# Optimization experiments

Hardware: AMD Instinct MI355X
Metric: run time of the kernel (lower is better)

Reference implementation:

```python
import jax, jax.numpy as jnp
import numpy as np

B, T, D = 128, 2048, 256
LAMDA = 0.5


def setup_inputs() -> dict:
    key = jax.random.key(0)
    ks = jax.random.split(key, 8)
    return {
        "sentiment": jax.random.normal(ks[0], (B, D), jnp.float32),
        "aspect": jax.random.normal(ks[1], (B, D), jnp.float32),
        "sentiment_memory": jax.random.normal(ks[2], (B, T, D), jnp.float32),
        "aspect_memory": jax.random.normal(ks[3], (B, T, D), jnp.float32),
        "mask": jnp.ones((B, T), jnp.float32),
        # MultiplicativeAttention params: rand(D,D)*0.2-0.1, bias zeros(1)
        "W_mul": jax.random.uniform(ks[4], (D, D), jnp.float32) * 0.2 - 0.1,
        "b_mul": jnp.zeros((1,), jnp.float32),
        # AdditiveAttention: Linear(2D, 1) -> weight vector [2D], bias [1]
        "w_ss": jax.random.normal(ks[5], (2 * D,), jnp.float32) * 0.02,
        "b_ss": jnp.zeros((1,), jnp.float32),
        "w_sa": jax.random.normal(ks[6], (2 * D,), jnp.float32) * 0.02,
        "b_sa": jnp.zeros((1,), jnp.float32),
    }


def _masked_norm(scores, mask):
    # exp(scores - max) * mask, normalized (matches torch branch exactly)
    s = scores - jnp.max(scores, axis=1, keepdims=True)
    e = jnp.exp(s) * mask
    return e / jnp.sum(e, axis=1, keepdims=True)


def _additive_attn(query, key_mem, w, b, mask):
    # Linear([key; query_repeated]) == key @ w_k + query @ w_q + b
    d = query.shape[-1]
    scores = key_mem @ w[:d] + (query @ w[d:])[:, None] + b[0]  # [B,T]
    return _masked_norm(scores, mask)


def reference(sentiment, aspect, sentiment_memory, aspect_memory, mask,
              W_mul, b_mul, w_ss, b_ss, w_sa, b_sa):
    # Multiplicative attention over aspect_memory (no mask -> plain softmax)
    mids = aspect @ W_mul.T                                        # W @ q, [B,D]
    a_scores = jnp.tanh(jnp.einsum('btd,bd->bt', aspect_memory, mids) + b_mul[0])
    aspect_attn = jax.nn.softmax(a_scores, axis=1)                 # [B,T]
    new_aspect = jnp.einsum('bt,btd->bd', aspect_attn, aspect_memory)  # [B,D]

    ss_attn = _additive_attn(sentiment, sentiment_memory, w_ss, b_ss, mask)
    sa_attn = _additive_attn(new_aspect, sentiment_memory, w_sa, b_sa, mask)
    s_attn = (1.0 - LAMDA) * ss_attn + LAMDA * sa_attn             # [B,T]

    sentiment_out = jnp.einsum('bt,btd->bd', s_attn, sentiment_memory)[:, None, :]  # [B,1,D]
    aspect_out = aspect + new_aspect                                # [B,D]
    return sentiment_out, aspect_out
```

## Files before the change

### kernel.cpp

```cpp
#include <hip/hip_runtime.h>
#include <math.h>

#define BB 128
#define TT 2048
#define DD 256
#define SPLIT 8
#define ROWS_PER_BLOCK (TT / SPLIT)
#define WAVES 4
#define ROWS_PER_WAVE (ROWS_PER_BLOCK / WAVES)

#define WS_MIDS 0
#define WS_P1ACC (WS_MIDS + BB * DD)
#define WS_P1SUM (WS_P1ACC + BB * SPLIT * DD)
#define WS_P2ACC_SS (WS_P1SUM + BB * SPLIT)
#define WS_P2ACC_SA (WS_P2ACC_SS + BB * SPLIT * DD)
#define WS_P2SUM_SS (WS_P2ACC_SA + BB * SPLIT * DD)
#define WS_P2SUM_SA (WS_P2SUM_SS + BB * SPLIT)

__device__ __forceinline__ float wave_reduce_add(float v) {
    #pragma unroll
    for (int off = 32; off > 0; off >>= 1)
        v += __shfl_xor(v, off, 64);
    return v;
}

__device__ __forceinline__ float dot4(const float4& a, const float4& b) {
    return a.x * b.x + a.y * b.y + a.z * b.z + a.w * b.w;
}

__device__ __forceinline__ float tanh_fast(float x) {
    float ax = fabsf(x);
    float t = __expf(-2.0f * ax);
    float th = (1.0f - t) / (1.0f + t);
    return copysignf(th, x);
}

__global__ __launch_bounds__(DD) void mids_kernel(
    const float* __restrict__ aspect, const float* __restrict__ W,
    float* __restrict__ ws)
{
    const int b = blockIdx.x;
    const int i = threadIdx.x;
    __shared__ float a[DD];
    a[i] = aspect[b * DD + i];
    __syncthreads();
    const float4* wrow = (const float4*)(W + (size_t)i * DD);
    float acc = 0.f;
    #pragma unroll 8
    for (int j4 = 0; j4 < DD / 4; ++j4) {
        float4 w4 = wrow[j4];
        acc += a[4 * j4 + 0] * w4.x + a[4 * j4 + 1] * w4.y +
               a[4 * j4 + 2] * w4.z + a[4 * j4 + 3] * w4.w;
    }
    ws[WS_MIDS + b * DD + i] = acc;
}

__global__ __launch_bounds__(256) void pass_kernel(
    const float* __restrict__ smem_g, const float* __restrict__ amem_g,
    const float* __restrict__ mask, const float* __restrict__ w_ss,
    const float* __restrict__ w_sa, const float* __restrict__ b_mul,
    float* __restrict__ ws)
{
    const int s = blockIdx.x;
    const int b = blockIdx.y;
    const int tid = threadIdx.x;
    const int wave = tid >> 6;
    const int lane = tid & 63;
    const int t0 = s * ROWS_PER_BLOCK + wave * ROWS_PER_WAVE;

    __shared__ __align__(16) float lds_acc[2 * WAVES * DD];
    __shared__ float lds_sum[2 * WAVES];

    if (blockIdx.z == 0) {
        const float4 m4 = *(const float4*)(ws + WS_MIDS + b * DD + lane * 4);
        const float bm = b_mul[0];
        const float* base = amem_g + ((size_t)b * TT + t0) * DD + lane * 4;
        float4 acc = make_float4(0.f, 0.f, 0.f, 0.f);
        float lsum = 0.f;
        for (int r = 0; r < ROWS_PER_WAVE; r += 2) {
            float4 v0 = *(const float4*)(base + (size_t)r * DD);
            float4 v1 = *(const float4*)(base + (size_t)(r + 1) * DD);
            float d0 = wave_reduce_add(dot4(v0, m4));
            float d1 = wave_reduce_add(dot4(v1, m4));
            float e0 = __expf(tanh_fast(d0 + bm));
            float e1 = __expf(tanh_fast(d1 + bm));
            lsum += e0 + e1;
            acc.x += e0 * v0.x + e1 * v1.x;
            acc.y += e0 * v0.y + e1 * v1.y;
            acc.z += e0 * v0.z + e1 * v1.z;
            acc.w += e0 * v0.w + e1 * v1.w;
        }
        ((float4*)(lds_acc + wave * DD))[lane] = acc;
        if (lane == 0) lds_sum[wave] = lsum;
        __syncthreads();
        float tot = lds_acc[0 * DD + tid] + lds_acc[1 * DD + tid] +
                    lds_acc[2 * DD + tid] + lds_acc[3 * DD + tid];
        ws[WS_P1ACC + (size_t)(b * SPLIT + s) * DD + tid] = tot;
        if (tid == 0)
            ws[WS_P1SUM + b * SPLIT + s] =
                lds_sum[0] + lds_sum[1] + lds_sum[2] + lds_sum[3];
    } else {
        const float4 wss4 = *(const float4*)(w_ss + lane * 4);
        const float4 wsa4 = *(const float4*)(w_sa + lane * 4);
        const float* base = smem_g + ((size_t)b * TT + t0) * DD + lane * 4;
        const float* mrow = mask + (size_t)b * TT + t0;
        float4 accss = make_float4(0.f, 0.f, 0.f, 0.f);
        float4 accsa = make_float4(0.f, 0.f, 0.f, 0.f);
        float lss = 0.f, lsa = 0.f;
        for (int r = 0; r < ROWS_PER_WAVE; r += 2) {
            float4 v0 = *(const float4*)(base + (size_t)r * DD);
            float4 v1 = *(const float4*)(base + (size_t)(r + 1) * DD);
            float m0 = mrow[r], m1 = mrow[r + 1];
            float dss0 = wave_reduce_add(dot4(v0, wss4));
            float dss1 = wave_reduce_add(dot4(v1, wss4));
            float dsa0 = wave_reduce_add(dot4(v0, wsa4));
            float dsa1 = wave_reduce_add(dot4(v1, wsa4));
            float ess0 = __expf(dss0) * m0, ess1 = __expf(dss1) * m1;
            float esa0 = __expf(dsa0) * m0, esa1 = __expf(dsa1) * m1;
            lss += ess0 + ess1;
            lsa += esa0 + esa1;
            accss.x += ess0 * v0.x + ess1 * v1.x;
            accss.y += ess0 * v0.y + ess1 * v1.y;
            accss.z += ess0 * v0.z + ess1 * v1.z;
            accss.w += ess0 * v0.w + ess1 * v1.w;
            accsa.x += esa0 * v0.x + esa1 * v1.x;
            accsa.y += esa0 * v0.y + esa1 * v1.y;
            accsa.z += esa0 * v0.z + esa1 * v1.z;
            accsa.w += esa0 * v0.w + esa1 * v1.w;
        }
        ((float4*)(lds_acc + wave * DD))[lane] = accss;
        ((float4*)(lds_acc + (WAVES + wave) * DD))[lane] = accsa;
        if (lane == 0) {
            lds_sum[wave] = lss;
            lds_sum[WAVES + wave] = lsa;
        }
        __syncthreads();
        float tot_ss = lds_acc[0 * DD + tid] + lds_acc[1 * DD + tid] +
                       lds_acc[2 * DD + tid] + lds_acc[3 * DD + tid];
        float tot_sa = lds_acc[(WAVES + 0) * DD + tid] + lds_acc[(WAVES + 1) * DD + tid] +
                       lds_acc[(WAVES + 2) * DD + tid] + lds_acc[(WAVES + 3) * DD + tid];
        ws[WS_P2ACC_SS + (size_t)(b * SPLIT + s) * DD + tid] = tot_ss;
        ws[WS_P2ACC_SA + (size_t)(b * SPLIT + s) * DD + tid] = tot_sa;
        if (tid == 0) {
            ws[WS_P2SUM_SS + b * SPLIT + s] =
                lds_sum[0] + lds_sum[1] + lds_sum[2] + lds_sum[3];
            ws[WS_P2SUM_SA + b * SPLIT + s] =
                lds_sum[4] + lds_sum[5] + lds_sum[6] + lds_sum[7];
        }
    }
}

__global__ __launch_bounds__(DD) void combine_kernel(
    const float* __restrict__ aspect, const float* __restrict__ ws,
    float* __restrict__ out)
{
    const int b = blockIdx.x;
    const int d = threadIdx.x;
    if (blockIdx.y == 0) {
        float acc = 0.f, l = 0.f;
        #pragma unroll
        for (int s = 0; s < SPLIT; ++s)
            acc += ws[WS_P1ACC + (size_t)(b * SPLIT + s) * DD + d];
        #pragma unroll
        for (int s = 0; s < SPLIT; ++s)
            l += ws[WS_P1SUM + b * SPLIT + s];
        out[BB * DD + b * DD + d] = aspect[b * DD + d] + acc / l;
    } else {
        float ass = 0.f, asa = 0.f, lss = 0.f, lsa = 0.f;
        #pragma unroll
        for (int s = 0; s < SPLIT; ++s) {
            ass += ws[WS_P2ACC_SS + (size_t)(b * SPLIT + s) * DD + d];
            asa += ws[WS_P2ACC_SA + (size_t)(b * SPLIT + s) * DD + d];
        }
        #pragma unroll
        for (int s = 0; s < SPLIT; ++s) {
            lss += ws[WS_P2SUM_SS + b * SPLIT + s];
            lsa += ws[WS_P2SUM_SA + b * SPLIT + s];
        }
        out[b * DD + d] = 0.5f * (ass / lss) + 0.5f * (asa / lsa);
    }
}

extern "C" void kernel_launch(void* const* d_in, const int* in_sizes, int n_in,
                              void* d_out, int out_size, void* d_ws, size_t ws_size,
                              hipStream_t stream) {
    (void)in_sizes; (void)n_in; (void)out_size; (void)ws_size;
    const float* aspect = (const float*)d_in[1];
    const float* smem   = (const float*)d_in[2];
    const float* amem   = (const float*)d_in[3];
    const float* mask   = (const float*)d_in[4];
    const float* W_mul  = (const float*)d_in[5];
    const float* b_mul  = (const float*)d_in[6];
    const float* w_ss   = (const float*)d_in[7];
    const float* w_sa   = (const float*)d_in[9];
    float* out = (float*)d_out;
    float* ws  = (float*)d_ws;

    mids_kernel<<<BB, DD, 0, stream>>>(aspect, W_mul, ws);
    pass_kernel<<<dim3(SPLIT, BB, 2), 256, 0, stream>>>(
        smem, amem, mask, w_ss, w_sa, b_mul, ws);
    combine_kernel<<<dim3(BB, 2), DD, 0, stream>>>(aspect, ws, out);
}
```

Measured before the change: 547.0 us.

## Split each wave into four 16-lane row groups with register prefetch

Each wave now handles four rows at once, one per 16-lane group, and each lane holds four float4 column slices. This cuts the per-row cross-lane reduction from six shuffle steps to four, shared across four rows. The row loop is fully unrolled with a next-row register prefetch so loads overlap compute. A final cross-group shuffle reduction merges the accumulators before the LDS write. Register pressure rises, especially in the sentiment branch with two sets of accumulators, which may lower occupancy.

```diff
diff --git a/kernel.cpp b/kernel.cpp
--- a/kernel.cpp
+++ b/kernel.cpp
@@ -7,7 +7,9 @@
 #define SPLIT 8
 #define ROWS_PER_BLOCK (TT / SPLIT)
 #define WAVES 4
-#define ROWS_PER_WAVE (ROWS_PER_BLOCK / WAVES)
+#define G 16
+#define RPB 4
+#define NB 16
 
 #define WS_MIDS 0
 #define WS_P1ACC (WS_MIDS + BB * DD)
@@ -17,13 +19,6 @@
 #define WS_P2SUM_SS (WS_P2ACC_SA + BB * SPLIT * DD)
 #define WS_P2SUM_SA (WS_P2SUM_SS + BB * SPLIT)
 
-__device__ __forceinline__ float wave_reduce_add(float v) {
-    #pragma unroll
-    for (int off = 32; off > 0; off >>= 1)
-        v += __shfl_xor(v, off, 64);
-    return v;
-}
-
 __device__ __forceinline__ float dot4(const float4& a, const float4& b) {
     return a.x * b.x + a.y * b.y + a.z * b.z + a.w * b.w;
 }
@@ -33,6 +28,15 @@
     float t = __expf(-2.0f * ax);
     float th = (1.0f - t) / (1.0f + t);
     return copysignf(th, x);
+}
+
+__device__ __forceinline__ float4 shfl_xor4(float4 v, int off) {
+    float4 r;
+    r.x = __shfl_xor(v.x, off, 64);
+    r.y = __shfl_xor(v.y, off, 64);
+    r.z = __shfl_xor(v.z, off, 64);
+    r.w = __shfl_xor(v.w, off, 64);
+    return r;
 }
 
 __global__ __launch_bounds__(DD) void mids_kernel(
@@ -66,31 +70,68 @@
     const int tid = threadIdx.x;
     const int wave = tid >> 6;
     const int lane = tid & 63;
-    const int t0 = s * ROWS_PER_BLOCK + wave * ROWS_PER_WAVE;
+    const int g = lane >> 4;
+    const int c = lane & 15;
+    const int t0 = s * ROWS_PER_BLOCK + wave * (RPB * NB);
 
     __shared__ __align__(16) float lds_acc[2 * WAVES * DD];
     __shared__ float lds_sum[2 * WAVES];
 
     if (blockIdx.z == 0) {
-        const float4 m4 = *(const float4*)(ws + WS_MIDS + b * DD + lane * 4);
+        float4 m4[4];
+        #pragma unroll
+        for (int j = 0; j < 4; ++j)
+            m4[j] = *(const float4*)(ws + WS_MIDS + b * DD + j * 64 + c * 4);
         const float bm = b_mul[0];
-        const float* base = amem_g + ((size_t)b * TT + t0) * DD + lane * 4;
-        float4 acc = make_float4(0.f, 0.f, 0.f, 0.f);
+        const float* base = amem_g + ((size_t)b * TT + t0 + g) * DD + c * 4;
+
+        float4 cur[4], nxt[4];
+        #pragma unroll
+        for (int j = 0; j < 4; ++j)
+            cur[j] = *(const float4*)(base + j * 64);
+
+        float4 acc[4];
+        #pragma unroll
+        for (int j = 0; j < 4; ++j) acc[j] = make_float4(0.f, 0.f, 0.f, 0.f);
         float lsum = 0.f;
-        for (int r = 0; r < ROWS_PER_WAVE; r += 2) {
-            float4 v0 = *(const float4*)(base + (size_t)r * DD);
-            float4 v1 = *(const float4*)(base + (size_t)(r + 1) * DD);
-            float d0 = wave_reduce_add(dot4(v0, m4));
-            float d1 = wave_reduce_add(dot4(v1, m4));
-            float e0 = __expf(tanh_fast(d0 + bm));
-            float e1 = __expf(tanh_fast(d1 + bm));
-            lsum += e0 + e1;
-            acc.x += e0 * v0.x + e1 * v1.x;
-            acc.y += e0 * v0.y + e1 * v1.y;
-            acc.z += e0 * v0.z + e1 * v1.z;
-            acc.w += e0 * v0.w + e1 * v1.w;
-        }
-        ((float4*)(lds_acc + wave * DD))[lane] = acc;
+
+        #pragma unroll
+        for (int i = 0; i < NB; ++i) {
+            if (i + 1 < NB) {
+                #pragma unroll
+                for (int j = 0; j < 4; ++j)
+                    nxt[j] = *(const float4*)(base + (size_t)(i + 1) * RPB * DD + j * 64);
+            }
+            float d = 0.f;
+            #pragma unroll
+            for (int j = 0; j < 4; ++j) d += dot4(cur[j], m4[j]);
+            #pragma unroll
+            for (int off = 1; off < G; off <<= 1)
+                d += __shfl_xor(d, off, 64);
+            float e = __expf(tanh_fast(d + bm));
+            lsum += e;
+            #pragma unroll
+            for (int j = 0; j < 4; ++j) {
+                acc[j].x += e * cur[j].x; acc[j].y += e * cur[j].y;
+                acc[j].z += e * cur[j].z; acc[j].w += e * cur[j].w;
+            }
+            #pragma unroll
+            for (int j = 0; j < 4; ++j) cur[j] = nxt[j];
+        }
+        #pragma unroll
+        for (int j = 0; j < 4; ++j) {
+            float4 o = shfl_xor4(acc[j], 16);
+            acc[j].x += o.x; acc[j].y += o.y; acc[j].z += o.z; acc[j].w += o.w;
+            o = shfl_xor4(acc[j], 32);
+            acc[j].x += o.x; acc[j].y += o.y; acc[j].z += o.z; acc[j].w += o.w;
+        }
+        lsum += __shfl_xor(lsum, 16, 64);
+        lsum += __shfl_xor(lsum, 32, 64);
+        if (g == 0) {
+            #pragma unroll
+            for (int j = 0; j < 4; ++j)
+                *(float4*)(lds_acc + wave * DD + j * 64 + c * 4) = acc[j];
+        }
         if (lane == 0) lds_sum[wave] = lsum;
         __syncthreads();
         float tot = lds_acc[0 * DD + tid] + lds_acc[1 * DD + tid] +
@@ -100,36 +141,83 @@
             ws[WS_P1SUM + b * SPLIT + s] =
                 lds_sum[0] + lds_sum[1] + lds_sum[2] + lds_sum[3];
     } else {
-        const float4 wss4 = *(const float4*)(w_ss + lane * 4);
-        const float4 wsa4 = *(const float4*)(w_sa + lane * 4);
-        const float* base = smem_g + ((size_t)b * TT + t0) * DD + lane * 4;
+        float4 wss4[4], wsa4[4];
+        #pragma unroll
+        for (int j = 0; j < 4; ++j) {
+            wss4[j] = *(const float4*)(w_ss + j * 64 + c * 4);
+            wsa4[j] = *(const float4*)(w_sa + j * 64 + c * 4);
+        }
+        const float* base = smem_g + ((size_t)b * TT + t0 + g) * DD + c * 4;
         const float* mrow = mask + (size_t)b * TT + t0;
-        float4 accss = make_float4(0.f, 0.f, 0.f, 0.f);
-        float4 accsa = make_float4(0.f, 0.f, 0.f, 0.f);
+
+        float4 cur[4], nxt[4];
+        #pragma unroll
+        for (int j = 0; j < 4; ++j)
+            cur[j] = *(const float4*)(base + j * 64);
+
+        float4 accss[4], accsa[4];
+        #pragma unroll
+        for (int j = 0; j < 4; ++j) {
+            accss[j] = make_float4(0.f, 0.f, 0.f, 0.f);
+            accsa[j] = make_float4(0.f, 0.f, 0.f, 0.f);
+        }
         float lss = 0.f, lsa = 0.f;
-        for (int r = 0; r < ROWS_PER_WAVE; r += 2) {
-            float4 v0 = *(const float4*)(base + (size_t)r * DD);
-            float4 v1 = *(const float4*)(base + (size_t)(r + 1) * DD);
-            float m0 = mrow[r], m1 = mrow[r + 1];
-            float dss0 = wave_reduce_add(dot4(v0, wss4));
-            float dss1 = wave_reduce_add(dot4(v1, wss4));
-            float dsa0 = wave_reduce_add(dot4(v0, wsa4));
-            float dsa1 = wave_reduce_add(dot4(v1, wsa4));
-            float ess0 = __expf(dss0) * m0, ess1 = __expf(dss1) * m1;
-            float esa0 = __expf(dsa0) * m0, esa1 = __expf(dsa1) * m1;
-            lss += ess0 + ess1;
-            lsa += esa0 + esa1;
-            accss.x += ess0 * v0.x + ess1 * v1.x;
-            accss.y += ess0 * v0.y + ess1 * v1.y;
-            accss.z += ess0 * v0.z + ess1 * v1.z;
-            accss.w += ess0 * v0.w + ess1 * v1.w;
-            accsa.x += esa0 * v0.x + esa1 * v1.x;
-            accsa.y += esa0 * v0.y + esa1 * v1.y;
-            accsa.z += esa0 * v0.z + esa1 * v1.z;
-            accsa.w += esa0 * v0.w + esa1 * v1.w;
-        }
-        ((float4*)(lds_acc + wave * DD))[lane] = accss;
-        ((float4*)(lds_acc + (WAVES + wave) * DD))[lane] = accsa;
+
+        #pragma unroll
+        for (int i = 0; i < NB; ++i) {
+            if (i + 1 < NB) {
+                #pragma unroll
+                for (int j = 0; j < 4; ++j)
+                    nxt[j] = *(const float4*)(base + (size_t)(i + 1) * RPB * DD + j * 64);
+            }
+            float dss = 0.f, dsa = 0.f;
+            #pragma unroll
+            for (int j = 0; j < 4; ++j) {
+                dss += dot4(cur[j], wss4[j]);
+                dsa += dot4(cur[j], wsa4[j]);
+            }
+            #pragma unroll
+            for (int off = 1; off < G; off <<= 1) {
+                dss += __shfl_xor(dss, off, 64);
+                dsa += __shfl_xor(dsa, off, 64);
+            }
+            float m = mrow[i * RPB + g];
+            float ess = __expf(dss) * m;
+            float esa = __expf(dsa) * m;
+            lss += ess;
+            lsa += esa;
+            #pragma unroll
+            for (int j = 0; j < 4; ++j) {
+                accss[j].x += ess * cur[j].x; accss[j].y += ess * cur[j].y;
+                accss[j].z += ess * cur[j].z; accss[j].w += ess * cur[j].w;
+                accsa[j].x += esa * cur[j].x; accsa[j].y += esa * cur[j].y;
+                accsa[j].z += esa * cur[j].z; accsa[j].w += esa * cur[j].w;
+            }
+            #pragma unroll
+            for (int j = 0; j < 4; ++j) cur[j] = nxt[j];
+        }
+        #pragma unroll
+        for (int j = 0; j < 4; ++j) {
+            float4 o = shfl_xor4(accss[j], 16);
+            accss[j].x += o.x; accss[j].y += o.y; accss[j].z += o.z; accss[j].w += o.w;
+            o = shfl_xor4(accss[j], 32);
+            accss[j].x += o.x; accss[j].y += o.y; accss[j].z += o.z; accss[j].w += o.w;
+            o = shfl_xor4(accsa[j], 16);
+            accsa[j].x += o.x; accsa[j].y += o.y; accsa[j].z += o.z; accsa[j].w += o.w;
+            o = shfl_xor4(accsa[j], 32);
+            accsa[j].x += o.x; accsa[j].y += o.y; accsa[j].z += o.z; accsa[j].w += o.w;
+        }
+        lss += __shfl_xor(lss, 16, 64);
+        lss += __shfl_xor(lss, 32, 64);
+        lsa += __shfl_xor(lsa, 16, 64);
+        lsa += __shfl_xor(lsa, 32, 64);
+        if (g == 0) {
+            #pragma unroll
+            for (int j = 0; j < 4; ++j) {
+                *(float4*)(lds_acc + wave * DD + j * 64 + c * 4) = accss[j];
+                *(float4*)(lds_acc + (WAVES + wave) * DD + j * 64 + c * 4) = accsa[j];
+            }
+        }
         if (lane == 0) {
             lds_sum[wave] = lss;
             lds_sum[WAVES + wave] = lsa;
```

After: 552.7 us. About the same (+1.0%).
